# Kernel optimization log

Hardware: AMD Instinct MI355X
Metric: run time of the kernel (lower is better)

## Reference

```python
import jax, jax.numpy as jnp
import numpy as np

N, E, D = 50000, 300000, 256
BN_EPS = 1e-5


def setup_inputs() -> dict:
    key = jax.random.key(0)
    ks = jax.random.split(key, 8)
    s = 1.0 / np.sqrt(D)
    return {
        'x': jax.random.normal(ks[0], (N, D), dtype=jnp.float32),
        'edge_index': jax.random.randint(ks[1], (2, E), 0, N, dtype=jnp.int64),
        'edge_attr': jax.random.normal(ks[2], (E, D), dtype=jnp.float32),
        'W1': jax.random.normal(ks[3], (D, D), dtype=jnp.float32) * s,
        'b1': jnp.zeros((D,), jnp.float32),
        'W2': jax.random.normal(ks[4], (D, D), dtype=jnp.float32) * s,
        'b2': jnp.zeros((D,), jnp.float32),
        'bn1_gamma': jnp.ones((D,), jnp.float32),
        'bn1_beta': jnp.zeros((D,), jnp.float32),
        'bn1_mean': jnp.zeros((D,), jnp.float32),
        'bn1_var': jnp.ones((D,), jnp.float32),
        'bn2_gamma': jnp.ones((D,), jnp.float32),
        'bn2_beta': jnp.zeros((D,), jnp.float32),
        'bn2_mean': jnp.zeros((D,), jnp.float32),
        'bn2_var': jnp.ones((D,), jnp.float32),
    }


def _bn(z, gamma, beta, mean, var):
    # eval-mode BatchNorm1d
    return (z - mean) * jax.lax.rsqrt(var + BN_EPS) * gamma + beta


def reference(x, edge_index, edge_attr, W1, b1, W2, b2,
              bn1_gamma, bn1_beta, bn1_mean, bn1_var,
              bn2_gamma, bn2_beta, bn2_mean, bn2_var):
    src, dst = edge_index[0], edge_index[1]
    # GINEConv message: relu(x_j + edge_attr), scatter-sum at destination
    msg = jax.nn.relu(x[src] + edge_attr)                      # [E, D]
    agg = jax.ops.segment_sum(msg, dst, num_segments=x.shape[0])  # [N, D]
    conv_out = x + agg            # (1+eps)*x + agg, eps=0; nn=Dropout is identity in eval
    h = x + conv_out              # residual: data.x + conv output
    # FFN: BN -> Linear -> GELU -> Linear
    f = _bn(h, bn1_gamma, bn1_beta, bn1_mean, bn1_var)
    f = jax.nn.gelu(f @ W1.T + b1, approximate=False)
    f = f @ W2.T + b2
    return _bn(h + f, bn2_gamma, bn2_beta, bn2_mean, bn2_var)
```

## Files before the change

kernel.cpp:

```cpp
#include <hip/hip_runtime.h>
#include <hip/hip_bf16.h>
#include <math.h>

#define D 256
#define D4 64
#define GSTRIDE 264

typedef __attribute__((ext_vector_type(8))) short bf16x8;
typedef __attribute__((ext_vector_type(4))) float f32x4;

__device__ inline unsigned short f2bf(float f) {
    union { float f; unsigned u; } v; v.f = f;
    unsigned r = v.u + 0x7fffu + ((v.u >> 16) & 1u);
    return (unsigned short)(r >> 16);
}
__device__ inline float bf2f(unsigned short u) {
    union { unsigned u; float f; } v; v.u = ((unsigned)u) << 16; return v.f;
}
__device__ inline float gelu_tanh(float t) {
    float z = 0.7978845608028654f * (t + 0.044715f * t * t * t);
    float e = __expf(2.f * z);
    return 0.5f * t * (2.f - 2.f / (e + 1.f));
}

__global__ __launch_bounds__(256) void k_prep(
    const float* __restrict__ W1, const float* __restrict__ W2,
    unsigned short* __restrict__ W1b, unsigned short* __restrict__ W2b,
    const float* g1, const float* be1, const float* m1, const float* v1,
    const float* g2, const float* be2, const float* m2, const float* v2,
    float* s1, float* sh1, float* r1, float* s2, float* sh2,
    int* counts, int* cursor, int N_)
{
    int i = blockIdx.x * 256 + threadIdx.x;
    if (i < D * D) {
        W1b[i] = f2bf(W1[i]);
        W2b[i] = f2bf(W2[i]);
    }
    if (i < N_) { counts[i] = 0; cursor[i] = 0; }
    if (i < D) {
        float sc1 = g1[i] * rsqrtf(v1[i] + 1e-5f);
        s1[i] = sc1; sh1[i] = be1[i] - m1[i] * sc1; r1[i] = 1.f / sc1;
        float sc2 = g2[i] * rsqrtf(v2[i] + 1e-5f);
        s2[i] = sc2; sh2[i] = be2[i] - m2[i] * sc2;
    }
}

__global__ __launch_bounds__(256) void k_hist(const int* __restrict__ ei, int* counts, int E_) {
    int e = blockIdx.x * 256 + threadIdx.x;
    if (e < E_) atomicAdd(&counts[ei[E_ + e]], 1);
}

__global__ __launch_bounds__(256) void k_scan1(const int* __restrict__ counts,
                                               int* offs, int* partials, int n) {
    __shared__ int tmp[256];
    int tid = threadIdx.x, i = blockIdx.x * 256 + tid;
    int v = (i < n) ? counts[i] : 0;
    tmp[tid] = v; __syncthreads();
    for (int d = 1; d < 256; d <<= 1) {
        int t = (tid >= d) ? tmp[tid - d] : 0;
        __syncthreads();
        tmp[tid] += t;
        __syncthreads();
    }
    if (i < n) offs[i] = tmp[tid] - v;
    if (tid == 255) partials[blockIdx.x] = tmp[255];
}

__global__ __launch_bounds__(256) void k_scan2(int* partials, int nb) {
    __shared__ int tmp[256];
    int tid = threadIdx.x;
    int v = (tid < nb) ? partials[tid] : 0;
    tmp[tid] = v; __syncthreads();
    for (int d = 1; d < 256; d <<= 1) {
        int t = (tid >= d) ? tmp[tid - d] : 0;
        __syncthreads();
        tmp[tid] += t;
        __syncthreads();
    }
    if (tid < nb) partials[tid] = tmp[tid] - v;
}

__global__ __launch_bounds__(256) void k_scan3(int* offs, const int* __restrict__ partials,
                                               int n, int E_) {
    int i = blockIdx.x * 256 + threadIdx.x;
    if (i < n) offs[i] += partials[blockIdx.x];
    if (i == 0) offs[n] = E_;
}

__global__ __launch_bounds__(256) void k_bucket(const int* __restrict__ ei,
                                                const int* __restrict__ offs,
                                                int* cursor, int2* sorted, int E_) {
    int e = blockIdx.x * 256 + threadIdx.x;
    if (e < E_) {
        int d = ei[E_ + e];
        int pos = offs[d] + atomicAdd(&cursor[d], 1);
        sorted[pos] = make_int2(ei[e], e);
    }
}

__global__ __launch_bounds__(256) void k_agg(
    const float4* __restrict__ x, const float4* __restrict__ ea,
    const int* __restrict__ offs, const int2* __restrict__ sorted,
    const float* __restrict__ s1, const float* __restrict__ sh1,
    ushort4* __restrict__ abf, int N_)
{
    int wave = threadIdx.x >> 6, lane = threadIdx.x & 63;
    int row = blockIdx.x * 4 + wave;
    if (row >= N_) return;
    float4 xv = x[(long)row * D4 + lane];
    float ax = 2.f * xv.x, ay = 2.f * xv.y, az = 2.f * xv.z, aw = 2.f * xv.w;
    int b = offs[row], en = offs[row + 1];
    for (int i = b; i < en; ++i) {
        int2 se = sorted[i];
        float4 sv = x[(long)se.x * D4 + lane];
        float4 av = ea[(long)se.y * D4 + lane];
        ax += fmaxf(sv.x + av.x, 0.f);
        ay += fmaxf(sv.y + av.y, 0.f);
        az += fmaxf(sv.z + av.z, 0.f);
        aw += fmaxf(sv.w + av.w, 0.f);
    }
    float4 sc = ((const float4*)s1)[lane];
    float4 sh = ((const float4*)sh1)[lane];
    ushort4 o;
    o.x = f2bf(ax * sc.x + sh.x);
    o.y = f2bf(ay * sc.y + sh.y);
    o.z = f2bf(az * sc.z + sh.z);
    o.w = f2bf(aw * sc.w + sh.w);
    abf[(long)row * D4 + lane] = o;
}

__global__ __launch_bounds__(256) void k_ffn(
    const unsigned short* __restrict__ A,
    const unsigned short* __restrict__ W1,
    const unsigned short* __restrict__ W2,
    const float* __restrict__ b1, const float* __restrict__ b2,
    const float* __restrict__ r1, const float* __restrict__ sh1,
    const float* __restrict__ s2, const float* __restrict__ sh2,
    float* __restrict__ out, int M)
{
    __shared__ __align__(16) unsigned short Gs[4][16][GSTRIDE];
    int wave = threadIdx.x >> 6, lane = threadIdx.x & 63;
    int m_base = (blockIdx.x * 4 + wave) * 16;
    if (m_base >= M) return;
    int l16 = lane & 15, quad = lane >> 4;

    const bf16x8* Arow = (const bf16x8*)(A + ((long)(m_base + l16) * D + quad * 8));
    bf16x8 frag[8];
#pragma unroll
    for (int s = 0; s < 8; ++s) frag[s] = Arow[s * 4];

#pragma unroll 2
    for (int nt = 0; nt < 16; ++nt) {
        int ncol = nt * 16 + l16;
        const bf16x8* Wrow = (const bf16x8*)(W1 + ((long)ncol * D + quad * 8));
        f32x4 acc0 = {0.f, 0.f, 0.f, 0.f};
        f32x4 acc1 = {0.f, 0.f, 0.f, 0.f};
#pragma unroll
        for (int s = 0; s < 8; s += 2) {
            acc0 = __builtin_amdgcn_mfma_f32_16x16x32_bf16(frag[s],     Wrow[s * 4],       acc0, 0, 0, 0);
            acc1 = __builtin_amdgcn_mfma_f32_16x16x32_bf16(frag[s + 1], Wrow[(s + 1) * 4], acc1, 0, 0, 0);
        }
        float b = b1[ncol];
#pragma unroll
        for (int r = 0; r < 4; ++r) {
            float t = acc0[r] + acc1[r] + b;
            Gs[wave][quad * 4 + r][ncol] = f2bf(gelu_tanh(t));
        }
    }

#pragma unroll
    for (int s = 0; s < 8; ++s)
        frag[s] = *(const bf16x8*)&Gs[wave][l16][quad * 8 + s * 32];

#pragma unroll 2
    for (int nt = 0; nt < 16; ++nt) {
        int ncol = nt * 16 + l16;
        const bf16x8* Wrow = (const bf16x8*)(W2 + ((long)ncol * D + quad * 8));
        f32x4 acc0 = {0.f, 0.f, 0.f, 0.f};
        f32x4 acc1 = {0.f, 0.f, 0.f, 0.f};
#pragma unroll
        for (int s = 0; s < 8; s += 2) {
            acc0 = __builtin_amdgcn_mfma_f32_16x16x32_bf16(frag[s],     Wrow[s * 4],       acc0, 0, 0, 0);
            acc1 = __builtin_amdgcn_mfma_f32_16x16x32_bf16(frag[s + 1], Wrow[(s + 1) * 4], acc1, 0, 0, 0);
        }
        float b = b2[ncol], rr = r1[ncol], sh = sh1[ncol];
        float c2 = s2[ncol], h2 = sh2[ncol];
#pragma unroll
        for (int r = 0; r < 4; ++r) {
            int row = m_base + quad * 4 + r;
            float f = acc0[r] + acc1[r] + b;
            float hv = (bf2f(A[(long)row * D + ncol]) - sh) * rr;
            out[(long)row * D + ncol] = (hv + f) * c2 + h2;
        }
    }
}

extern "C" void kernel_launch(void* const* d_in, const int* in_sizes, int n_in,
                              void* d_out, int out_size, void* d_ws, size_t ws_size,
                              hipStream_t stream) {
    const float* x   = (const float*)d_in[0];
    const int*   ei  = (const int*)d_in[1];
    const float* ea  = (const float*)d_in[2];
    const float* W1  = (const float*)d_in[3];
    const float* b1  = (const float*)d_in[4];
    const float* W2  = (const float*)d_in[5];
    const float* b2  = (const float*)d_in[6];
    const float* g1  = (const float*)d_in[7];
    const float* be1 = (const float*)d_in[8];
    const float* m1  = (const float*)d_in[9];
    const float* v1  = (const float*)d_in[10];
    const float* g2  = (const float*)d_in[11];
    const float* be2 = (const float*)d_in[12];
    const float* m2  = (const float*)d_in[13];
    const float* v2  = (const float*)d_in[14];
    float* out = (float*)d_out;

    int N_ = in_sizes[0] / D;
    int E_ = in_sizes[2] / D;

    char* ws = (char*)d_ws;
    size_t off = 0;
    unsigned short* abf = (unsigned short*)(ws + off);  off += (size_t)N_ * D * 2;
    unsigned short* W1b = (unsigned short*)(ws + off);  off += (size_t)D * D * 2;
    unsigned short* W2b = (unsigned short*)(ws + off);  off += (size_t)D * D * 2;
    float* s1  = (float*)(ws + off); off += D * 4;
    float* sh1 = (float*)(ws + off); off += D * 4;
    float* r1  = (float*)(ws + off); off += D * 4;
    float* s2  = (float*)(ws + off); off += D * 4;
    float* sh2 = (float*)(ws + off); off += D * 4;
    int* counts   = (int*)(ws + off); off += (size_t)N_ * 4;
    int* cursor   = (int*)(ws + off); off += (size_t)N_ * 4;
    int* offs     = (int*)(ws + off); off += (size_t)(N_ + 1) * 4;
    int* partials = (int*)(ws + off); off += 256 * 4;
    int2* sorted  = (int2*)(ws + off); off += (size_t)E_ * 8;

    int nblkN = (N_ + 255) / 256;
    int nblkE = (E_ + 255) / 256;

    k_prep<<<(D * D + 255) / 256, 256, 0, stream>>>(W1, W2, W1b, W2b,
        g1, be1, m1, v1, g2, be2, m2, v2, s1, sh1, r1, s2, sh2, counts, cursor, N_);
    k_hist<<<nblkE, 256, 0, stream>>>(ei, counts, E_);
    k_scan1<<<nblkN, 256, 0, stream>>>(counts, offs, partials, N_);
    k_scan2<<<1, 256, 0, stream>>>(partials, nblkN);
    k_scan3<<<nblkN, 256, 0, stream>>>(offs, partials, N_, E_);
    k_bucket<<<nblkE, 256, 0, stream>>>(ei, offs, cursor, sorted, E_);
    k_agg<<<(N_ + 3) / 4, 256, 0, stream>>>((const float4*)x, (const float4*)ea,
        offs, sorted, s1, sh1, (ushort4*)abf, N_);

    int mtiles = (N_ + 15) / 16;
    k_ffn<<<(mtiles + 3) / 4, 256, 0, stream>>>(abf, W1b, W2b, b1, b2,
        r1, sh1, s2, sh2, out, N_);
}
```

Measured before the change: 655.4 us.

## Fuse edge aggregation into FFN kernel with block-shared 16-row tiles

Merges the gather/aggregate kernel with the MFMA FFN kernel so each block aggregates 16 rows into LDS and then all four waves split the output columns of both GEMMs, removing the bf16 intermediate round trip through global memory. The bucket cursor is also initialised to the row offsets in the scan kernel, which drops one load per edge in the bucketing pass. In exchange it adds block-wide barriers, and a slow high-degree row now stalls the whole block's GEMM. Each wave also computes only a quarter of the columns, so per-wave MFMA work falls while the number of blocks rises fourfold.

```diff
diff --git a/kernel.cpp b/kernel.cpp
--- a/kernel.cpp
+++ b/kernel.cpp
@@ -4,7 +4,7 @@
 
 #define D 256
 #define D4 64
-#define GSTRIDE 264
+#define GS 264
 
 typedef __attribute__((ext_vector_type(8))) short bf16x8;
 typedef __attribute__((ext_vector_type(4))) float f32x4;
@@ -29,14 +29,14 @@
     const float* g1, const float* be1, const float* m1, const float* v1,
     const float* g2, const float* be2, const float* m2, const float* v2,
     float* s1, float* sh1, float* r1, float* s2, float* sh2,
-    int* counts, int* cursor, int N_)
+    int* counts, int N_)
 {
     int i = blockIdx.x * 256 + threadIdx.x;
     if (i < D * D) {
         W1b[i] = f2bf(W1[i]);
         W2b[i] = f2bf(W2[i]);
     }
-    if (i < N_) { counts[i] = 0; cursor[i] = 0; }
+    if (i < N_) counts[i] = 0;
     if (i < D) {
         float sc1 = g1[i] * rsqrtf(v1[i] + 1e-5f);
         s1[i] = sc1; sh1[i] = be1[i] - m1[i] * sc1; r1[i] = 1.f / sc1;
@@ -80,78 +80,83 @@
     if (tid < nb) partials[tid] = tmp[tid] - v;
 }
 
-__global__ __launch_bounds__(256) void k_scan3(int* offs, const int* __restrict__ partials,
+__global__ __launch_bounds__(256) void k_scan3(int* offs, int* cursor,
+                                               const int* __restrict__ partials,
                                                int n, int E_) {
     int i = blockIdx.x * 256 + threadIdx.x;
-    if (i < n) offs[i] += partials[blockIdx.x];
+    if (i < n) {
+        int v = offs[i] + partials[blockIdx.x];
+        offs[i] = v;
+        cursor[i] = v;
+    }
     if (i == 0) offs[n] = E_;
 }
 
 __global__ __launch_bounds__(256) void k_bucket(const int* __restrict__ ei,
-                                                const int* __restrict__ offs,
                                                 int* cursor, int2* sorted, int E_) {
     int e = blockIdx.x * 256 + threadIdx.x;
     if (e < E_) {
         int d = ei[E_ + e];
-        int pos = offs[d] + atomicAdd(&cursor[d], 1);
+        int pos = atomicAdd(&cursor[d], 1);
         sorted[pos] = make_int2(ei[e], e);
     }
 }
 
-__global__ __launch_bounds__(256) void k_agg(
+__global__ __launch_bounds__(256) void k_fused(
     const float4* __restrict__ x, const float4* __restrict__ ea,
     const int* __restrict__ offs, const int2* __restrict__ sorted,
     const float* __restrict__ s1, const float* __restrict__ sh1,
-    ushort4* __restrict__ abf, int N_)
-{
-    int wave = threadIdx.x >> 6, lane = threadIdx.x & 63;
-    int row = blockIdx.x * 4 + wave;
-    if (row >= N_) return;
-    float4 xv = x[(long)row * D4 + lane];
-    float ax = 2.f * xv.x, ay = 2.f * xv.y, az = 2.f * xv.z, aw = 2.f * xv.w;
-    int b = offs[row], en = offs[row + 1];
-    for (int i = b; i < en; ++i) {
-        int2 se = sorted[i];
-        float4 sv = x[(long)se.x * D4 + lane];
-        float4 av = ea[(long)se.y * D4 + lane];
-        ax += fmaxf(sv.x + av.x, 0.f);
-        ay += fmaxf(sv.y + av.y, 0.f);
-        az += fmaxf(sv.z + av.z, 0.f);
-        aw += fmaxf(sv.w + av.w, 0.f);
-    }
-    float4 sc = ((const float4*)s1)[lane];
-    float4 sh = ((const float4*)sh1)[lane];
-    ushort4 o;
-    o.x = f2bf(ax * sc.x + sh.x);
-    o.y = f2bf(ay * sc.y + sh.y);
-    o.z = f2bf(az * sc.z + sh.z);
-    o.w = f2bf(aw * sc.w + sh.w);
-    abf[(long)row * D4 + lane] = o;
-}
-
-__global__ __launch_bounds__(256) void k_ffn(
-    const unsigned short* __restrict__ A,
-    const unsigned short* __restrict__ W1,
-    const unsigned short* __restrict__ W2,
+    const float* __restrict__ r1,
+    const unsigned short* __restrict__ W1, const unsigned short* __restrict__ W2,
     const float* __restrict__ b1, const float* __restrict__ b2,
-    const float* __restrict__ r1, const float* __restrict__ sh1,
     const float* __restrict__ s2, const float* __restrict__ sh2,
     float* __restrict__ out, int M)
 {
-    __shared__ __align__(16) unsigned short Gs[4][16][GSTRIDE];
+    __shared__ __align__(16) unsigned short As[16][GS];
+    __shared__ __align__(16) unsigned short Gsm[16][GS];
+
     int wave = threadIdx.x >> 6, lane = threadIdx.x & 63;
-    int m_base = (blockIdx.x * 4 + wave) * 16;
-    if (m_base >= M) return;
+    int m_base = blockIdx.x * 16;
+
+    float4 sc1v = ((const float4*)s1)[lane];
+    float4 sh1v = ((const float4*)sh1)[lane];
+#pragma unroll
+    for (int rr = 0; rr < 4; ++rr) {
+        int tr = wave * 4 + rr;
+        int row = m_base + tr;
+        if (row < M) {
+            float4 xv = x[(long)row * D4 + lane];
+            float ax = 2.f * xv.x, ay = 2.f * xv.y, az = 2.f * xv.z, aw = 2.f * xv.w;
+            int b = offs[row], en = offs[row + 1];
+            for (int i = b; i < en; ++i) {
+                int2 se = sorted[i];
+                float4 sv = x[(long)se.x * D4 + lane];
+                float4 av = ea[(long)se.y * D4 + lane];
+                ax += fmaxf(sv.x + av.x, 0.f);
+                ay += fmaxf(sv.y + av.y, 0.f);
+                az += fmaxf(sv.z + av.z, 0.f);
+                aw += fmaxf(sv.w + av.w, 0.f);
+            }
+            ushort4 o;
+            o.x = f2bf(ax * sc1v.x + sh1v.x);
+            o.y = f2bf(ay * sc1v.y + sh1v.y);
+            o.z = f2bf(az * sc1v.z + sh1v.z);
+            o.w = f2bf(aw * sc1v.w + sh1v.w);
+            *(ushort4*)&As[tr][lane * 4] = o;
+        }
+    }
+    __syncthreads();
+
     int l16 = lane & 15, quad = lane >> 4;
 
-    const bf16x8* Arow = (const bf16x8*)(A + ((long)(m_base + l16) * D + quad * 8));
     bf16x8 frag[8];
 #pragma unroll
-    for (int s = 0; s < 8; ++s) frag[s] = Arow[s * 4];
-
-#pragma unroll 2
-    for (int nt = 0; nt < 16; ++nt) {
-        int ncol = nt * 16 + l16;
+    for (int s = 0; s < 8; ++s)
+        frag[s] = *(const bf16x8*)&As[l16][quad * 8 + s * 32];
+
+#pragma unroll
+    for (int t = 0; t < 4; ++t) {
+        int ncol = (wave * 4 + t) * 16 + l16;
         const bf16x8* Wrow = (const bf16x8*)(W1 + ((long)ncol * D + quad * 8));
         f32x4 acc0 = {0.f, 0.f, 0.f, 0.f};
         f32x4 acc1 = {0.f, 0.f, 0.f, 0.f};
@@ -163,18 +168,19 @@
         float b = b1[ncol];
 #pragma unroll
         for (int r = 0; r < 4; ++r) {
-            float t = acc0[r] + acc1[r] + b;
-            Gs[wave][quad * 4 + r][ncol] = f2bf(gelu_tanh(t));
-        }
-    }
+            float v = acc0[r] + acc1[r] + b;
+            Gsm[quad * 4 + r][ncol] = f2bf(gelu_tanh(v));
+        }
+    }
+    __syncthreads();
 
 #pragma unroll
     for (int s = 0; s < 8; ++s)
-        frag[s] = *(const bf16x8*)&Gs[wave][l16][quad * 8 + s * 32];
-
-#pragma unroll 2
-    for (int nt = 0; nt < 16; ++nt) {
-        int ncol = nt * 16 + l16;
+        frag[s] = *(const bf16x8*)&Gsm[l16][quad * 8 + s * 32];
+
+#pragma unroll
+    for (int t = 0; t < 4; ++t) {
+        int ncol = (wave * 4 + t) * 16 + l16;
         const bf16x8* Wrow = (const bf16x8*)(W2 + ((long)ncol * D + quad * 8));
         f32x4 acc0 = {0.f, 0.f, 0.f, 0.f};
         f32x4 acc1 = {0.f, 0.f, 0.f, 0.f};
@@ -183,14 +189,17 @@
             acc0 = __builtin_amdgcn_mfma_f32_16x16x32_bf16(frag[s],     Wrow[s * 4],       acc0, 0, 0, 0);
             acc1 = __builtin_amdgcn_mfma_f32_16x16x32_bf16(frag[s + 1], Wrow[(s + 1) * 4], acc1, 0, 0, 0);
         }
-        float b = b2[ncol], rr = r1[ncol], sh = sh1[ncol];
+        float b = b2[ncol], rr1 = r1[ncol], sh = sh1[ncol];
         float c2 = s2[ncol], h2 = sh2[ncol];
 #pragma unroll
         for (int r = 0; r < 4; ++r) {
-            int row = m_base + quad * 4 + r;
-            float f = acc0[r] + acc1[r] + b;
-            float hv = (bf2f(A[(long)row * D + ncol]) - sh) * rr;
-            out[(long)row * D + ncol] = (hv + f) * c2 + h2;
+            int tr = quad * 4 + r;
+            int row = m_base + tr;
+            if (row < M) {
+                float f = acc0[r] + acc1[r] + b;
+                float hv = (bf2f(As[tr][ncol]) - sh) * rr1;
+                out[(long)row * D + ncol] = (hv + f) * c2 + h2;
+            }
         }
     }
 }
@@ -220,7 +229,6 @@
 
     char* ws = (char*)d_ws;
     size_t off = 0;
-    unsigned short* abf = (unsigned short*)(ws + off);  off += (size_t)N_ * D * 2;
     unsigned short* W1b = (unsigned short*)(ws + off);  off += (size_t)D * D * 2;
     unsigned short* W2b = (unsigned short*)(ws + off);  off += (size_t)D * D * 2;
     float* s1  = (float*)(ws + off); off += D * 4;
@@ -238,16 +246,14 @@
     int nblkE = (E_ + 255) / 256;
 
     k_prep<<<(D * D + 255) / 256, 256, 0, stream>>>(W1, W2, W1b, W2b,
-        g1, be1, m1, v1, g2, be2, m2, v2, s1, sh1, r1, s2, sh2, counts, cursor, N_);
+        g1, be1, m1, v1, g2, be2, m2, v2, s1, sh1, r1, s2, sh2, counts, N_);
     k_hist<<<nblkE, 256, 0, stream>>>(ei, counts, E_);
     k_scan1<<<nblkN, 256, 0, stream>>>(counts, offs, partials, N_);
     k_scan2<<<1, 256, 0, stream>>>(partials, nblkN);
-    k_scan3<<<nblkN, 256, 0, stream>>>(offs, partials, N_, E_);
-    k_bucket<<<nblkE, 256, 0, stream>>>(ei, offs, cursor, sorted, E_);
-    k_agg<<<(N_ + 3) / 4, 256, 0, stream>>>((const float4*)x, (const float4*)ea,
-        offs, sorted, s1, sh1, (ushort4*)abf, N_);
+    k_scan3<<<nblkN, 256, 0, stream>>>(offs, cursor, partials, N_, E_);
+    k_bucket<<<nblkE, 256, 0, stream>>>(ei, cursor, sorted, E_);
 
     int mtiles = (N_ + 15) / 16;
-    k_ffn<<<(mtiles + 3) / 4, 256, 0, stream>>>(abf, W1b, W2b, b1, b2,
-        r1, sh1, s2, sh2, out, N_);
-}
+    k_fused<<<mtiles, 256, 0, stream>>>((const float4*)x, (const float4*)ea,
+        offs, sorted, s1, sh1, r1, W1b, W2b, b1, b2, s2, sh2, out, N_);
+}
```

Measured after the change: 652.3 us. Within noise of the previous version (-0.5%).
